# Optimization experiments

Measured on AMD Instinct MI355X. Metric: run time of the kernel, lower is better.

The kernel has to match this reference:

```python
import jax, jax.numpy as jnp
import numpy as np

B, S, D = 8, 2048, 512
H, DK, DV = 8, 64, 64


def setup_inputs() -> dict:
    key = jax.random.key(0)
    ks = jax.random.split(key, 12)
    def xavier(k, shape):
        fan_in, fan_out = shape[0], shape[1]
        std = (2.0 / (fan_in + fan_out)) ** 0.5
        return jax.random.normal(k, shape, dtype=jnp.float32) * std
    return {
        "Q": jax.random.normal(ks[0], (B, S, D), dtype=jnp.float32),
        "K": jax.random.normal(ks[1], (B, S, D), dtype=jnp.float32),
        "V": jax.random.normal(ks[2], (B, S, D), dtype=jnp.float32),
        "W_q": xavier(ks[3], (D, H * DK)),
        "W_k": xavier(ks[4], (D, H * DK)),
        "W_v": xavier(ks[5], (D, H * DV)),
        "W_o": xavier(ks[6], (H * DV, D)),
        "W1": xavier(ks[7], (D, D)),  # linear1.weight, stored [out, in]
        "b1": jnp.zeros((D,), dtype=jnp.float32),
        "W2": xavier(ks[8], (D, D)),  # linear2.weight
        "b2": jnp.zeros((D,), dtype=jnp.float32),
    }


def reference(Q, K, V, W_q, W_k, W_v, W_o, W1, b1, W2, b2):
    eps = 1e-6
    bsz, q_len, _ = Q.shape
    # project and split heads: [B, S, H, dk]
    Qh = (Q @ W_q).reshape(bsz, q_len, H, DK)
    Kh = (K @ W_k).reshape(bsz, q_len, H, DK)
    Vh = (V @ W_v).reshape(bsz, q_len, H, DV)
    temperature = DK ** 0.5
    # scores: [B, H, Sq, Sk] (full O(N^2) matrix, as in original)
    scores = jnp.einsum('bqhd,bkhd->bhqk', Qh, Kh) / (temperature + eps)
    probs = jax.nn.softmax(scores, axis=-1)  # dropout = identity (eval)
    V_att = jnp.einsum('bhqk,bkhd->bqhd', probs, Vh).reshape(bsz, q_len, H * DV)
    attn_out = V_att @ W_o  # dropout = identity
    X = Q + attn_out
    # FFN: linear2(relu(linear1(X))); torch Linear: x @ W.T + b
    ffn = jax.nn.relu(X @ W1.T + b1) @ W2.T + b2
    return ffn + X
```

## Files before the change

kernel.cpp:

```cpp
#include <hip/hip_runtime.h>
#include <stdint.h>

typedef __bf16 bf16;
typedef bf16 bf16x8 __attribute__((ext_vector_type(8)));
typedef bf16 bf16x4 __attribute__((ext_vector_type(4)));
typedef float f32x2 __attribute__((ext_vector_type(2)));
typedef float f32x4 __attribute__((ext_vector_type(4)));
typedef float f32x16 __attribute__((ext_vector_type(16)));

#define AS1 __attribute__((address_space(1)))
#define AS3 __attribute__((address_space(3)))

__device__ __forceinline__ void gll16(const void* g, void* l) {
    __builtin_amdgcn_global_load_lds((const AS1 unsigned int*)g,
                                     (AS3 unsigned int*)l, 16, 0, 0);
}

__device__ __forceinline__ bf16 f2bf(float x) { return (bf16)x; }

__device__ __forceinline__ float fexp2(float x) { return __builtin_amdgcn_exp2f(x); }

#define QSCALE_LOG2E 0.18033685757f

__global__ void k_castw(const float* __restrict__ Wq, const float* __restrict__ Wk,
                        const float* __restrict__ Wv, const float* __restrict__ Wo,
                        const float* __restrict__ W1, const float* __restrict__ W2,
                        bf16* __restrict__ oq, bf16* __restrict__ ok, bf16* __restrict__ ov,
                        bf16* __restrict__ oo, bf16* __restrict__ o1, bf16* __restrict__ o2)
{
    const int z = blockIdx.y;
    const int idx = blockIdx.x * 256 + threadIdx.x;
    const float* src = z == 0 ? Wq : z == 1 ? Wk : z == 2 ? Wv : z == 3 ? Wo : z == 4 ? W1 : W2;
    bf16* dst = z == 0 ? oq : z == 1 ? ok : z == 2 ? ov : z == 3 ? oo : z == 4 ? o1 : o2;
    if (z < 4) {
        const int n = idx >> 9, k = idx & 511;
        dst[idx] = f2bf(src[(k << 9) + n]);
    } else {
        dst[idx] = f2bf(src[idx]);
    }
}

__device__ __forceinline__ void gemm_core(const bf16* __restrict__ A,
                                          const bf16* __restrict__ Bt,
                                          const int K, bf16* As, bf16* Bs,
                                          const int bm, const int bn,
                                          f32x4 acc[4][4])
{
    const int tid  = threadIdx.x;
    const int lane = tid & 63;
    const int wave = tid >> 6;
    const int g    = lane >> 4;
    const int l15  = lane & 15;
    const int wm   = (wave >> 1) * 64;
    const int wn   = (wave & 1) * 64;

    const int srow = tid >> 2;
    const int sk   = (tid & 3) * 8;
    const size_t aoff0 = (size_t)(bm + srow) * K + sk;
    const size_t aoff1 = (size_t)(bm + 64 + srow) * K + sk;
    const size_t boff0 = (size_t)(bn + srow) * K + sk;
    const size_t boff1 = (size_t)(bn + 64 + srow) * K + sk;
    char* asb = (char*)As + wave * 1024;
    char* bsb = (char*)Bs + wave * 1024;

    for (int kt = 0; kt < K; kt += 32) {
        __syncthreads();
        gll16(A + aoff0 + kt, asb);
        gll16(A + aoff1 + kt, asb + 4096);
        gll16(Bt + boff0 + kt, bsb);
        gll16(Bt + boff1 + kt, bsb + 4096);
        __syncthreads();
        bf16x8 af[4], bfv[4];
#pragma unroll
        for (int mi = 0; mi < 4; ++mi)
            af[mi] = *(const bf16x8*)&As[(wm + mi * 16 + l15) * 32 + g * 8];
#pragma unroll
        for (int ni = 0; ni < 4; ++ni)
            bfv[ni] = *(const bf16x8*)&Bs[(wn + ni * 16 + l15) * 32 + g * 8];
#pragma unroll
        for (int mi = 0; mi < 4; ++mi)
#pragma unroll
            for (int ni = 0; ni < 4; ++ni)
                acc[mi][ni] = __builtin_amdgcn_mfma_f32_16x16x32_bf16(
                    af[mi], bfv[ni], acc[mi][ni], 0, 0, 0);
    }
}

template<int EPI>
__global__ __launch_bounds__(256)
void k_gemm(const bf16* __restrict__ A, const bf16* __restrict__ Bt,
            const float* __restrict__ bias, const float* __restrict__ residf,
            const bf16* __restrict__ residb,
            float* __restrict__ Cf, bf16* __restrict__ Cb,
            int M, int N, int K)
{
    __shared__ bf16 As[128 * 32];
    __shared__ bf16 Bs[128 * 32];
    const int bm = blockIdx.y * 128, bn = blockIdx.x * 128;
    f32x4 acc[4][4] = {};
    gemm_core(A, Bt, K, As, Bs, bm, bn, acc);

    const int tid  = threadIdx.x;
    const int lane = tid & 63;
    const int wave = tid >> 6;
    const int g    = lane >> 4;
    const int l15  = lane & 15;
    const int wm   = (wave >> 1) * 64;
    const int wn   = (wave & 1) * 64;
    const int col0 = bn + wn + l15;
#pragma unroll
    for (int ni = 0; ni < 4; ++ni) {
        const int col = col0 + ni * 16;
        float bv = 0.f;
        if constexpr (EPI == 2 || EPI == 3) bv = bias[col];
#pragma unroll
        for (int mi = 0; mi < 4; ++mi) {
#pragma unroll
            for (int r = 0; r < 4; ++r) {
                const int row = bm + wm + mi * 16 + 4 * g + r;
                const size_t idx = (size_t)row * N + col;
                float v = acc[mi][ni][r];
                if constexpr (EPI == 1) {
                    Cb[idx] = f2bf(v + residf[idx]);
                } else if constexpr (EPI == 2) {
                    Cb[idx] = f2bf(fmaxf(v + bv, 0.f));
                } else {
                    Cf[idx] = v + bv + (float)residb[idx];
                }
            }
        }
    }
}

__global__ __launch_bounds__(256)
void k_proj(const float* __restrict__ Qf, const float* __restrict__ Kf, const float* __restrict__ Vf,
            const bf16* __restrict__ BQ, const bf16* __restrict__ BK, const bf16* __restrict__ BV,
            bf16* __restrict__ OQ, bf16* __restrict__ OK_, bf16* __restrict__ OV)
{
    __shared__ char SMRAW[24576];
    bf16* Bs = (bf16*)(SMRAW + 16384);

    const int dd = blockIdx.x;
    const int x = dd & 7, q = dd >> 3;
    const int bnb = q & 3;
    const int tt = x * 48 + (q >> 2);
    const int z  = tt >> 7;
    const int bm = (tt & 127) * 128;
    const int bn = bnb * 128;

    const float* A = z == 0 ? Qf : z == 1 ? Kf : Vf;
    const bf16* Bt = z == 0 ? BQ : z == 1 ? BK : BV;
    bf16* Cb       = z == 0 ? OQ : z == 1 ? OK_ : OV;

    const int tid  = threadIdx.x;
    const int lane = tid & 63;
    const int wave = tid >> 6;
    const int g    = lane >> 4;
    const int l15  = lane & 15;
    const int wm   = (wave >> 1) * 64;
    const int wn   = (wave & 1) * 64;

    const int krow = tid >> 3, kc = tid & 7;
    const size_t aoff = (size_t)(bm + krow) * 512 + ((kc ^ (krow & 7)) << 2);
    const int srow = tid >> 2;
    const int sk   = (tid & 3) * 8;
    const size_t boff0 = (size_t)(bn + srow) * 512 + sk;
    const size_t boff1 = (size_t)(bn + 64 + srow) * 512 + sk;
    char* bsb = (char*)Bs + wave * 1024;

    f32x4 acc[4][4] = {};

    for (int kt = 0; kt < 512; kt += 32) {
        __syncthreads();
#pragma unroll
        for (int j = 0; j < 4; ++j)
            gll16(A + aoff + j * 16384 + kt, SMRAW + j * 4096 + tid * 16);
        gll16(Bt + boff0 + kt, bsb);
        gll16(Bt + boff1 + kt, bsb + 4096);
        __syncthreads();
        bf16x8 af[4];
        bf16x8 bfv[4];
#pragma unroll
        for (int mi = 0; mi < 4; ++mi) {
            const int row = wm + mi * 16 + l15;
            const int r7 = row & 7;
            float4 lo = *(const float4*)(SMRAW + row * 128 + (((2 * g) ^ r7) << 4));
            float4 hi = *(const float4*)(SMRAW + row * 128 + (((2 * g + 1) ^ r7) << 4));
            af[mi][0] = f2bf(lo.x); af[mi][1] = f2bf(lo.y);
            af[mi][2] = f2bf(lo.z); af[mi][3] = f2bf(lo.w);
            af[mi][4] = f2bf(hi.x); af[mi][5] = f2bf(hi.y);
            af[mi][6] = f2bf(hi.z); af[mi][7] = f2bf(hi.w);
        }
#pragma unroll
        for (int ni = 0; ni < 4; ++ni)
            bfv[ni] = *(const bf16x8*)&Bs[(wn + ni * 16 + l15) * 32 + g * 8];
#pragma unroll
        for (int mi = 0; mi < 4; ++mi)
#pragma unroll
            for (int ni = 0; ni < 4; ++ni)
                acc[mi][ni] = __builtin_amdgcn_mfma_f32_16x16x32_bf16(
                    af[mi], bfv[ni], acc[mi][ni], 0, 0, 0);
    }

    const int bb = bm >> 11;
    const int s0 = bm & 2047;
    __syncthreads();
#pragma unroll
    for (int p = 0; p < 2; ++p) {
        if ((wave >> 1) == p) {
            if (z == 0) {
#pragma unroll
                for (int ni = 0; ni < 4; ++ni) {
                    const int col = wn + ni * 16 + l15;
                    const int hh = col >> 6, dk = col & 63;
                    char* img = SMRAW + hh * 8192;
#pragma unroll
                    for (int mi = 0; mi < 4; ++mi)
#pragma unroll
                        for (int r = 0; r < 4; ++r) {
                            const int sl = mi * 16 + 4 * g + r;
                            *(bf16*)(img + (sl * 64 + dk) * 2) =
                                f2bf(acc[mi][ni][r] * QSCALE_LOG2E);
                        }
                }
            } else if (z == 1) {
#pragma unroll
                for (int ni = 0; ni < 4; ++ni) {
                    const int col = wn + ni * 16 + l15;
                    const int hh = col >> 6, dk = col & 63;
                    const int ks = dk >> 4, h2 = (dk >> 3) & 1, e = dk & 7;
                    char* img = SMRAW + hh * 8192;
#pragma unroll
                    for (int mi = 0; mi < 4; ++mi)
#pragma unroll
                        for (int r = 0; r < 4; ++r) {
                            const int sl = mi * 16 + 4 * g + r;
                            const int t2 = sl >> 5, ql = sl & 31;
                            *(bf16*)(img + (((t2 * 4 + ks) * 64 + h2 * 32 + ql) * 8 + e) * 2) =
                                f2bf(acc[mi][ni][r]);
                        }
                }
            } else {
#pragma unroll
                for (int ni = 0; ni < 4; ++ni) {
                    const int col = wn + ni * 16 + l15;
                    const int hh = col >> 6, dv = col & 63;
                    const int dvt = dv >> 5, ql = dv & 31;
                    char* img = SMRAW + hh * 8192;
#pragma unroll
                    for (int mi = 0; mi < 4; ++mi)
#pragma unroll
                        for (int r = 0; r < 4; ++r) {
                            const int sl = mi * 16 + 4 * g + r;
                            const int ktile = sl >> 4, kk = sl & 15;
                            const int h2 = (kk >> 2) & 1;
                            const int e = (kk & 3) | ((kk >> 3) << 2);
                            *(bf16*)(img + (((dvt * 4 + ktile) * 64 + h2 * 32 + ql) * 8 + e) * 2) =
                                f2bf(acc[mi][ni][r]);
                        }
                }
            }
        }
        __syncthreads();
        {
            const int hh = tid >> 7, t = tid & 127;
            const int hg = (bn >> 6) + hh;
            const size_t a0 = (size_t)(bb * 8 + hg) * 131072;
            const size_t slab = (z == 0) ? a0 + (size_t)(s0 + p * 64) * 64
                                         : a0 + (size_t)((s0 >> 6) + p) * 4096;
            const char* img = SMRAW + hh * 8192;
#pragma unroll
            for (int i = 0; i < 4; ++i) {
                const int G = i * 128 + t;
                bf16x8 vv = *(const bf16x8*)(img + G * 16);
                *(bf16x8*)&Cb[slab + (size_t)G * 8] = vv;
            }
        }
        if (p == 0) __syncthreads();
    }
}

__global__ __launch_bounds__(256, 2)
void k_attn(const bf16* __restrict__ Qp, const bf16* __restrict__ Khp,
            const bf16* __restrict__ Vtp, bf16* __restrict__ O)
{
    __shared__ bf16 smem[16384];
    const int tid = threadIdx.x;
    const int l   = tid & 63;
    const int w   = tid >> 6;
    const int h   = l >> 5;
    const int ql  = l & 31;
    const int d   = blockIdx.x;
    const int bh  = ((d >> 6) << 3) | (d & 7);
    const int qt  = (d >> 3) & 7;
    const size_t base = (size_t)bh * 131072;
    const int q0 = qt * 256 + w * 64;
    const int loff = l * 16;

    bf16x8 qfA[4], qfB[4];
#pragma unroll
    for (int ks = 0; ks < 4; ++ks) {
        qfA[ks] = *(const bf16x8*)&Qp[base + (size_t)(q0 + ql) * 64 + ks * 16 + h * 8];
        qfB[ks] = *(const bf16x8*)&Qp[base + (size_t)(q0 + 32 + ql) * 64 + ks * 16 + h * 8];
    }

    f32x16 oA0 = {}, oA1 = {}, oB0 = {}, oB1 = {};
    float lrunA = 0.f, lrunB = 0.f;

    const bf16* ksrc = Khp + base + tid * 8;
    const bf16* vsrc = Vtp + base + tid * 8;
    char* kb0 = (char*)smem;
    char* kb1 = (char*)smem + 16384;
    const int wdst = w * 1024;

    auto stage = [&](int kvt, char* kb) {
        const bf16* ks = ksrc + kvt * 4096;
        const bf16* vs = vsrc + kvt * 4096;
        gll16(ks,        kb + wdst);
        gll16(ks + 2048, kb + 4096 + wdst);
        gll16(vs,        kb + 8192 + wdst);
        gll16(vs + 2048, kb + 12288 + wdst);
    };

    auto compute = [&](const char* kb) {
        f32x16 sA0 = {}, sA1 = {}, sB0 = {}, sB1 = {};
        __builtin_amdgcn_s_setprio(1);
#pragma unroll
        for (int ks = 0; ks < 4; ++ks) {
            bf16x8 a0 = *(const bf16x8*)(kb + ks * 1024 + loff);
            bf16x8 a1 = *(const bf16x8*)(kb + 4096 + ks * 1024 + loff);
            sA0 = __builtin_amdgcn_mfma_f32_32x32x16_bf16(a0, qfA[ks], sA0, 0, 0, 0);
            sB0 = __builtin_amdgcn_mfma_f32_32x32x16_bf16(a0, qfB[ks], sB0, 0, 0, 0);
            sA1 = __builtin_amdgcn_mfma_f32_32x32x16_bf16(a1, qfA[ks], sA1, 0, 0, 0);
            sB1 = __builtin_amdgcn_mfma_f32_32x32x16_bf16(a1, qfB[ks], sB1, 0, 0, 0);
        }
        __builtin_amdgcn_s_setprio(0);

        f32x2 pA = {0.f, 0.f}, pB = {0.f, 0.f};
#pragma unroll
        for (int r = 0; r < 16; r += 2) {
            sA0[r]     = fexp2(sA0[r]);
            sA0[r + 1] = fexp2(sA0[r + 1]);
            sA1[r]     = fexp2(sA1[r]);
            sA1[r + 1] = fexp2(sA1[r + 1]);
            pA += (f32x2){sA0[r], sA0[r + 1]};
            pA += (f32x2){sA1[r], sA1[r + 1]};
        }
#pragma unroll
        for (int r = 0; r < 16; r += 2) {
            sB0[r]     = fexp2(sB0[r]);
            sB0[r + 1] = fexp2(sB0[r + 1]);
            sB1[r]     = fexp2(sB1[r]);
            sB1[r + 1] = fexp2(sB1[r + 1]);
            pB += (f32x2){sB0[r], sB0[r + 1]};
            pB += (f32x2){sB1[r], sB1[r + 1]};
        }
        lrunA += pA[0] + pA[1];
        lrunB += pB[0] + pB[1];

        bf16x8 pbA[4], pbB[4];
#pragma unroll
        for (int j = 0; j < 4; ++j) {
            const int ofs = 8 * (j & 1);
#pragma unroll
            for (int e = 0; e < 8; ++e) {
                pbA[j][e] = f2bf((j & 2) ? sA1[ofs + e] : sA0[ofs + e]);
                pbB[j][e] = f2bf((j & 2) ? sB1[ofs + e] : sB0[ofs + e]);
            }
        }

        const char* vr = kb + 8192;
        __builtin_amdgcn_s_setprio(1);
#pragma unroll
        for (int j = 0; j < 4; ++j) {
            bf16x8 a0 = *(const bf16x8*)(vr + j * 1024 + loff);
            bf16x8 a1 = *(const bf16x8*)(vr + 4096 + j * 1024 + loff);
            oA0 = __builtin_amdgcn_mfma_f32_32x32x16_bf16(a0, pbA[j], oA0, 0, 0, 0);
            oB0 = __builtin_amdgcn_mfma_f32_32x32x16_bf16(a0, pbB[j], oB0, 0, 0, 0);
            oA1 = __builtin_amdgcn_mfma_f32_32x32x16_bf16(a1, pbA[j], oA1, 0, 0, 0);
            oB1 = __builtin_amdgcn_mfma_f32_32x32x16_bf16(a1, pbB[j], oB1, 0, 0, 0);
        }
        __builtin_amdgcn_s_setprio(0);
    };

    stage(0, kb0);
    __syncthreads();
    for (int kvt = 0; kvt < 32; kvt += 2) {
        if (kvt + 1 < 32) stage(kvt + 1, kb1);
        compute(kb0);
        __syncthreads();
        if (kvt + 2 < 32) stage(kvt + 2, kb0);
        compute(kb1);
        __syncthreads();
    }

    char* ot = (char*)smem + w * 4096;
    const int qr = l >> 1;
    const int dh4 = (l & 1) * 4;
    auto epi = [&](const f32x16& e0, const f32x16& e1, float lr, int qg) {
        lr += __shfl_xor(lr, 32);
        const float inv = 1.f / lr;
#pragma unroll
        for (int dvt = 0; dvt < 2; ++dvt) {
#pragma unroll
            for (int r = 0; r < 16; ++r) {
                const int dv = dvt * 32 + (r & 3) + 8 * (r >> 2) + 4 * h;
                const float val = (dvt ? e1[r] : e0[r]) * inv;
                *(bf16*)(ot + ql * 128 + ((((dv >> 3) ^ (ql & 7)) << 4) | ((dv & 7) << 1))) = f2bf(val);
            }
        }
        const size_t ob = ((size_t)(bh >> 3) * 2048 + qg + qr) * 512 + (bh & 7) * 64 + (size_t)dh4 * 8;
#pragma unroll
        for (int B = 0; B < 4; ++B) {
            bf16x8 v = *(const bf16x8*)(ot + qr * 128 + (((dh4 + B) ^ (qr & 7)) << 4));
            *(bf16x8*)&O[ob + B * 8] = v;
        }
    };
    epi(oA0, oA1, lrunA, q0);
    epi(oB0, oB1, lrunB, q0 + 32);
}

extern "C" void kernel_launch(void* const* d_in, const int* in_sizes, int n_in,
                              void* d_out, int out_size, void* d_ws, size_t ws_size,
                              hipStream_t stream)
{
    const float* Q  = (const float*)d_in[0];
    const float* K  = (const float*)d_in[1];
    const float* V  = (const float*)d_in[2];
    const float* Wq = (const float*)d_in[3];
    const float* Wk = (const float*)d_in[4];
    const float* Wv = (const float*)d_in[5];
    const float* Wo = (const float*)d_in[6];
    const float* W1 = (const float*)d_in[7];
    const float* b1 = (const float*)d_in[8];
    const float* W2 = (const float*)d_in[9];
    const float* b2 = (const float*)d_in[10];
    float* out = (float*)d_out;

    const int M = 8 * 2048;
    const size_t TN = (size_t)M * 512;
    const int WN = 512 * 512;

    char* ws = (char*)d_ws;
    bf16* Qhp  = (bf16*)ws;
    bf16* Khp  = Qhp + TN;
    bf16* Vtp  = Khp + TN;
    bf16* Vatt = Vtp + TN;
    bf16* H1   = Vatt + TN;
    bf16* Xbf  = H1 + TN;
    bf16* Wqt  = Xbf + TN;
    bf16* Wkt  = Wqt + WN;
    bf16* Wvt  = Wkt + WN;
    bf16* Wot  = Wvt + WN;
    bf16* W1b  = Wot + WN;
    bf16* W2b  = W1b + WN;

    k_castw<<<dim3(1024, 6), 256, 0, stream>>>(Wq, Wk, Wv, Wo, W1, W2,
                                               Wqt, Wkt, Wvt, Wot, W1b, W2b);

    k_proj<<<1536, 256, 0, stream>>>(Q, K, V, Wqt, Wkt, Wvt,
                                     Qhp, Khp, Vtp);

    k_attn<<<512, 256, 0, stream>>>(Qhp, Khp, Vtp, Vatt);

    dim3 gg(4, 128);
    k_gemm<1><<<gg, 256, 0, stream>>>(Vatt, Wot, nullptr, Q, nullptr, nullptr, Xbf, M, 512, 512);
    k_gemm<2><<<gg, 256, 0, stream>>>(Xbf, W1b, b1, nullptr, nullptr, nullptr, H1, M, 512, 512);
    k_gemm<3><<<gg, 256, 0, stream>>>(H1, W2b, b2, nullptr, Xbf, out, nullptr, M, 512, 512);
}
```

Baseline: 191.7 us.

## Triple-buffer k_proj LDS loads with vmcnt-based prefetch pipeline

Rewrites the projection GEMM main loop to prefetch two K-steps ahead into three rotating LDS buffers. Explicit s_waitcnt vmcnt counts and raw barriers replace the two __syncthreads per iteration. The aim is to hide global-to-LDS load latency behind MFMA work. LDS use per block grows from 24 KB to 72 KB, which may cut occupancy.

```diff
diff --git a/kernel.cpp b/kernel.cpp
--- a/kernel.cpp
+++ b/kernel.cpp
@@ -19,6 +19,8 @@
 __device__ __forceinline__ bf16 f2bf(float x) { return (bf16)x; }
 
 __device__ __forceinline__ float fexp2(float x) { return __builtin_amdgcn_exp2f(x); }
+
+#define WAITV(N) asm volatile("s_waitcnt vmcnt(" #N ")" ::: "memory")
 
 #define QSCALE_LOG2E 0.18033685757f
 
@@ -137,8 +139,7 @@
             const bf16* __restrict__ BQ, const bf16* __restrict__ BK, const bf16* __restrict__ BV,
             bf16* __restrict__ OQ, bf16* __restrict__ OK_, bf16* __restrict__ OV)
 {
-    __shared__ char SMRAW[24576];
-    bf16* Bs = (bf16*)(SMRAW + 16384);
+    __shared__ char SMRAW[73728];
 
     const int dd = blockIdx.x;
     const int x = dd & 7, q = dd >> 3;
@@ -166,26 +167,26 @@
     const int sk   = (tid & 3) * 8;
     const size_t boff0 = (size_t)(bn + srow) * 512 + sk;
     const size_t boff1 = (size_t)(bn + 64 + srow) * 512 + sk;
-    char* bsb = (char*)Bs + wave * 1024;
 
     f32x4 acc[4][4] = {};
 
-    for (int kt = 0; kt < 512; kt += 32) {
-        __syncthreads();
+    auto stageF = [&](int s, char* buf) {
+        const int kt = s * 32;
 #pragma unroll
         for (int j = 0; j < 4; ++j)
-            gll16(A + aoff + j * 16384 + kt, SMRAW + j * 4096 + tid * 16);
-        gll16(Bt + boff0 + kt, bsb);
-        gll16(Bt + boff1 + kt, bsb + 4096);
-        __syncthreads();
-        bf16x8 af[4];
-        bf16x8 bfv[4];
+            gll16(A + aoff + j * 16384 + kt, buf + j * 4096 + tid * 16);
+        gll16(Bt + boff0 + kt, buf + 16384 + wave * 1024);
+        gll16(Bt + boff1 + kt, buf + 16384 + 4096 + wave * 1024);
+    };
+
+    auto computeF = [&](const char* buf) {
+        bf16x8 af[4], bfv[4];
 #pragma unroll
         for (int mi = 0; mi < 4; ++mi) {
             const int row = wm + mi * 16 + l15;
             const int r7 = row & 7;
-            float4 lo = *(const float4*)(SMRAW + row * 128 + (((2 * g) ^ r7) << 4));
-            float4 hi = *(const float4*)(SMRAW + row * 128 + (((2 * g + 1) ^ r7) << 4));
+            float4 lo = *(const float4*)(buf + row * 128 + (((2 * g) ^ r7) << 4));
+            float4 hi = *(const float4*)(buf + row * 128 + (((2 * g + 1) ^ r7) << 4));
             af[mi][0] = f2bf(lo.x); af[mi][1] = f2bf(lo.y);
             af[mi][2] = f2bf(lo.z); af[mi][3] = f2bf(lo.w);
             af[mi][4] = f2bf(hi.x); af[mi][5] = f2bf(hi.y);
@@ -193,13 +194,32 @@
         }
 #pragma unroll
         for (int ni = 0; ni < 4; ++ni)
-            bfv[ni] = *(const bf16x8*)&Bs[(wn + ni * 16 + l15) * 32 + g * 8];
+            bfv[ni] = *(const bf16x8*)(buf + 16384 +
+                        ((wn + ni * 16 + l15) * 32 + g * 8) * 2);
 #pragma unroll
         for (int mi = 0; mi < 4; ++mi)
 #pragma unroll
             for (int ni = 0; ni < 4; ++ni)
                 acc[mi][ni] = __builtin_amdgcn_mfma_f32_16x16x32_bf16(
                     af[mi], bfv[ni], acc[mi][ni], 0, 0, 0);
+    };
+
+    stageF(0, SMRAW);
+    stageF(1, SMRAW + 24576);
+#pragma unroll
+    for (int t = 0; t < 16; ++t) {
+        if (t + 2 < 16) {
+            stageF(t + 2, SMRAW + ((t + 2) % 3) * 24576);
+            WAITV(12);
+        } else if (t + 1 < 16) {
+            WAITV(6);
+        } else {
+            WAITV(0);
+        }
+        __builtin_amdgcn_s_barrier();
+        __builtin_amdgcn_sched_barrier(0);
+        computeF(SMRAW + (t % 3) * 24576);
+        __builtin_amdgcn_s_barrier();
     }
 
     const int bb = bm >> 11;
```

After: 193.8 us. Within noise of the previous version (+1.1%).

## Tile weight-cast transpose through LDS and split projection into per-tensor templated launches

Applied to the files above, without the earlier changes.

The weight cast/transpose kernel now stages 64x64 tiles in shared memory, so global reads are float4-coalesced and 16 elements are processed per thread instead of doing one strided scalar read per thread. The fused Q/K/V projection launch is split into three templated launches, which removes the runtime branching on z and makes the epilogue selection compile-time. The trade-off is two extra kernel launches and the loss of concurrent overlap between the three projections inside a single grid.

```diff
diff --git a/kernel.cpp b/kernel.cpp
--- a/kernel.cpp
+++ b/kernel.cpp
@@ -28,15 +28,36 @@
                         bf16* __restrict__ oq, bf16* __restrict__ ok, bf16* __restrict__ ov,
                         bf16* __restrict__ oo, bf16* __restrict__ o1, bf16* __restrict__ o2)
 {
+    __shared__ bf16 L[64][65];
     const int z = blockIdx.y;
-    const int idx = blockIdx.x * 256 + threadIdx.x;
+    const int t = threadIdx.x;
     const float* src = z == 0 ? Wq : z == 1 ? Wk : z == 2 ? Wv : z == 3 ? Wo : z == 4 ? W1 : W2;
     bf16* dst = z == 0 ? oq : z == 1 ? ok : z == 2 ? ov : z == 3 ? oo : z == 4 ? o1 : o2;
     if (z < 4) {
-        const int n = idx >> 9, k = idx & 511;
-        dst[idx] = f2bf(src[(k << 9) + n]);
+        const int tr = blockIdx.x >> 3, tc = blockIdx.x & 7;
+        const int r = t >> 2, c0 = (t & 3) * 16;
+#pragma unroll
+        for (int i = 0; i < 4; ++i) {
+            float4 v = *(const float4*)(src + (size_t)(tr * 64 + r) * 512 + tc * 64 + c0 + i * 4);
+            L[r][c0 + i * 4 + 0] = f2bf(v.x);
+            L[r][c0 + i * 4 + 1] = f2bf(v.y);
+            L[r][c0 + i * 4 + 2] = f2bf(v.z);
+            L[r][c0 + i * 4 + 3] = f2bf(v.w);
+        }
+        __syncthreads();
+        const int c2 = t >> 2, r0 = (t & 3) * 16;
+        bf16* d = dst + (size_t)(tc * 64 + c2) * 512 + tr * 64 + r0;
+#pragma unroll
+        for (int i = 0; i < 16; ++i) d[i] = L[r0 + i][c2];
     } else {
-        dst[idx] = f2bf(src[idx]);
+        const size_t base = (size_t)blockIdx.x * 4096 + t * 16;
+#pragma unroll
+        for (int i = 0; i < 4; ++i) {
+            float4 v = *(const float4*)(src + base + i * 4);
+            bf16x4 o;
+            o[0] = f2bf(v.x); o[1] = f2bf(v.y); o[2] = f2bf(v.z); o[3] = f2bf(v.w);
+            *(bf16x4*)(dst + base + i * 4) = o;
+        }
     }
 }
 
@@ -132,26 +153,19 @@
     }
 }
 
+template<int Z>
 __global__ __launch_bounds__(256)
-void k_proj(const float* __restrict__ Qf, const float* __restrict__ Kf, const float* __restrict__ Vf,
-            const bf16* __restrict__ BQ, const bf16* __restrict__ BK, const bf16* __restrict__ BV,
-            bf16* __restrict__ OQ, bf16* __restrict__ OK_, bf16* __restrict__ OV)
+void k_projZ(const float* __restrict__ A, const bf16* __restrict__ Bt,
+             bf16* __restrict__ Cb)
 {
     __shared__ char SMRAW[24576];
-    bf16* Bs = (bf16*)(SMRAW + 16384);
 
     const int dd = blockIdx.x;
     const int x = dd & 7, q = dd >> 3;
-    const int bnb = q & 3;
-    const int tt = x * 48 + (q >> 2);
-    const int z  = tt >> 7;
-    const int bm = (tt & 127) * 128;
-    const int bn = bnb * 128;
-
-    const float* A = z == 0 ? Qf : z == 1 ? Kf : Vf;
-    const bf16* Bt = z == 0 ? BQ : z == 1 ? BK : BV;
-    bf16* Cb       = z == 0 ? OQ : z == 1 ? OK_ : OV;
-
+    const int bn = (q & 3) * 128;
+    const int bm = (x * 16 + (q >> 2)) * 128;
+
+    bf16* Bs = (bf16*)(SMRAW + 16384);
     const int tid  = threadIdx.x;
     const int lane = tid & 63;
     const int wave = tid >> 6;
@@ -166,7 +180,6 @@
     const int sk   = (tid & 3) * 8;
     const size_t boff0 = (size_t)(bn + srow) * 512 + sk;
     const size_t boff1 = (size_t)(bn + 64 + srow) * 512 + sk;
-    char* bsb = (char*)Bs + wave * 1024;
 
     f32x4 acc[4][4] = {};
 
@@ -175,11 +188,10 @@
 #pragma unroll
         for (int j = 0; j < 4; ++j)
             gll16(A + aoff + j * 16384 + kt, SMRAW + j * 4096 + tid * 16);
-        gll16(Bt + boff0 + kt, bsb);
-        gll16(Bt + boff1 + kt, bsb + 4096);
-        __syncthreads();
-        bf16x8 af[4];
-        bf16x8 bfv[4];
+        gll16(Bt + boff0 + kt, (char*)Bs + wave * 1024);
+        gll16(Bt + boff1 + kt, (char*)Bs + wave * 1024 + 4096);
+        __syncthreads();
+        bf16x8 af[4], bfv[4];
 #pragma unroll
         for (int mi = 0; mi < 4; ++mi) {
             const int row = wm + mi * 16 + l15;
@@ -208,7 +220,7 @@
 #pragma unroll
     for (int p = 0; p < 2; ++p) {
         if ((wave >> 1) == p) {
-            if (z == 0) {
+            if constexpr (Z == 0) {
 #pragma unroll
                 for (int ni = 0; ni < 4; ++ni) {
                     const int col = wn + ni * 16 + l15;
@@ -223,7 +235,7 @@
                                 f2bf(acc[mi][ni][r] * QSCALE_LOG2E);
                         }
                 }
-            } else if (z == 1) {
+            } else if constexpr (Z == 1) {
 #pragma unroll
                 for (int ni = 0; ni < 4; ++ni) {
                     const int col = wn + ni * 16 + l15;
@@ -266,7 +278,7 @@
             const int hh = tid >> 7, t = tid & 127;
             const int hg = (bn >> 6) + hh;
             const size_t a0 = (size_t)(bb * 8 + hg) * 131072;
-            const size_t slab = (z == 0) ? a0 + (size_t)(s0 + p * 64) * 64
+            const size_t slab = (Z == 0) ? a0 + (size_t)(s0 + p * 64) * 64
                                          : a0 + (size_t)((s0 >> 6) + p) * 4096;
             const char* img = SMRAW + hh * 8192;
 #pragma unroll
@@ -455,11 +467,12 @@
     bf16* W1b  = Wot + WN;
     bf16* W2b  = W1b + WN;
 
-    k_castw<<<dim3(1024, 6), 256, 0, stream>>>(Wq, Wk, Wv, Wo, W1, W2,
-                                               Wqt, Wkt, Wvt, Wot, W1b, W2b);
-
-    k_proj<<<1536, 256, 0, stream>>>(Q, K, V, Wqt, Wkt, Wvt,
-                                     Qhp, Khp, Vtp);
+    k_castw<<<dim3(64, 6), 256, 0, stream>>>(Wq, Wk, Wv, Wo, W1, W2,
+                                             Wqt, Wkt, Wvt, Wot, W1b, W2b);
+
+    k_projZ<0><<<512, 256, 0, stream>>>(Q, Wqt, Qhp);
+    k_projZ<1><<<512, 256, 0, stream>>>(K, Wkt, Khp);
+    k_projZ<2><<<512, 256, 0, stream>>>(V, Wvt, Vtp);
 
     k_attn<<<512, 256, 0, stream>>>(Qhp, Khp, Vtp, Vatt);
 
```

Result: slower. 204.7 us (+6.8%).
